# Optimization experiments

Measured on AMD Instinct MI355X. Metric: run time of the kernel, lower is better.

## Reference

```python
import jax, jax.numpy as jnp
import numpy as np
from jax import lax

V = 33          # n_vertices
B, H, W = 8, 1024, 1024
RES = 256       # backbone input resolution
N_FEATS = 128 * 8 * 8  # 8192


def setup_inputs() -> dict:
    key = jax.random.key(0)
    ks = jax.random.split(key, 16)
    inp = {"x": jax.random.uniform(ks[0], (B, 3, H, W), jnp.float32)}
    chans = [(3, 16), (16, 32), (32, 64), (64, 128), (128, 128)]
    for i, (ci, co) in enumerate(chans):
        inp[f"cw{i}"] = jax.random.normal(ks[1 + i], (co, ci, 3, 3), jnp.float32) / float(np.sqrt(ci * 9))
        inp[f"cb{i}"] = jnp.zeros((co,), jnp.float32)
    for i, c in enumerate([16, 32, 64, 128]):
        inp[f"g{i}"] = 1.0 + 0.02 * jax.random.normal(ks[6 + i], (c,), jnp.float32)  # InstanceNorm affine init
        inp[f"be{i}"] = jnp.zeros((c,), jnp.float32)
    inp["wg_w"] = 0.01 * jax.random.normal(ks[10], (3, N_FEATS), jnp.float32)
    inp["wg_b"] = jnp.ones((3,), jnp.float32)  # init_weights: ones bias
    # basis LUT bank: rank 0 = identity LUT (meshgrid, flip(0)), other ranks small noise
    grid = jnp.stack(jnp.meshgrid(*[jnp.arange(V, dtype=jnp.float32)] * 3, indexing="ij"), 0) / (V - 1)
    identity = jnp.flip(grid, 0).reshape(1, -1)          # [1, 3*V^3]
    rest = 0.01 * jax.random.normal(ks[11], (2, 3 * V ** 3), jnp.float32)
    inp["lut_w"] = jnp.concatenate([identity, rest], 0).T  # [3*V^3, n_ranks]
    inp["vertices"] = jnp.broadcast_to(jnp.arange(V, dtype=jnp.float32) / (V - 1), (3, V))[None]  # [1,3,V]
    return inp


def _conv(x, w, b, stride=2):
    y = lax.conv_general_dilated(x, w, (stride, stride), ((1, 1), (1, 1)),
                                 dimension_numbers=("NCHW", "OIHW", "NCHW"))
    return y + b[None, :, None, None]


def _inorm(x, g, be, eps=1e-5):
    m = x.mean((2, 3), keepdims=True)
    v = x.var((2, 3), keepdims=True)  # biased, matches torch InstanceNorm
    return (x - m) / jnp.sqrt(v + eps) * g[None, :, None, None] + be[None, :, None, None]


def _leaky(x):
    return jnp.where(x >= 0, x, 0.2 * x)


def _backbone(x, cws, cbs, gs, bes):
    h = jax.image.resize(x, (x.shape[0], 3, RES, RES), "bilinear")
    for i in range(4):  # Conv -> LeakyReLU -> InstanceNorm
        h = _inorm(_leaky(_conv(h, cws[i], cbs[i])), gs[i], bes[i])
    h = _leaky(_conv(h, cws[4], cbs[4]))  # last block, no norm; dropout = identity (eval)
    return h.reshape(x.shape[0], -1)


def _ailut(img, luts, vertices):
    # img [B,3,H,W], luts [B,3,V,V,V] (axes: out_ch, b, g, r), vertices [1,3,V]
    Bn, Vn = img.shape[0], vertices.shape[-1]
    verts = jnp.broadcast_to(vertices, (Bn, 3, Vn))
    q = img.reshape(Bn * 3, -1)
    vflat = verts.reshape(Bn * 3, Vn)
    idx = jax.vmap(lambda v, qq: jnp.searchsorted(v, qq, side="right"))(vflat, q) - 1
    idx = jnp.clip(idx, 0, Vn - 2).reshape(Bn, 3, -1)       # bin index per (b, color, pixel)
    lo = jnp.take_along_axis(verts, idx, axis=2)
    hi = jnp.take_along_axis(verts, idx + 1, axis=2)
    d = (img.reshape(Bn, 3, -1) - lo) / (hi - lo)           # fractional offset
    ir, ig, ib = idx[:, 0], idx[:, 1], idx[:, 2]
    dr, dg, db = d[:, 0], d[:, 1], d[:, 2]
    lflat = luts.reshape(Bn, 3, Vn ** 3)
    out = jnp.zeros_like(d)
    for ob in (0, 1):
        for og in (0, 1):
            for orr in (0, 1):
                w = ((db if ob else 1 - db) * (dg if og else 1 - dg) * (dr if orr else 1 - dr))
                lin = ((ib + ob) * Vn + (ig + og)) * Vn + (ir + orr)
                vals = jnp.take_along_axis(lflat, lin[:, None, :], axis=2)  # [B,3,N]
                out = out + w[:, None, :] * vals
    return out.reshape(img.shape)


def reference(x, cw0, cw1, cw2, cw3, cw4, cb0, cb1, cb2, cb3, cb4,
              g0, g1, g2, g3, be0, be1, be2, be3, wg_w, wg_b, lut_w, vertices):
    codes = _backbone(x, [cw0, cw1, cw2, cw3, cw4], [cb0, cb1, cb2, cb3, cb4],
                      [g0, g1, g2, g3], [be0, be1, be2, be3])   # [B, 8192]
    weights = codes @ wg_w.T + wg_b                              # [B, 3]
    luts = (weights @ lut_w.T).reshape(x.shape[0], 3, V, V, V)   # [B,3,V,V,V]
    outs = _ailut(x, luts, vertices)
    return outs, weights, luts, vertices
```

## Files before the change

kernel.cpp:

```cpp
#include <hip/hip_runtime.h>
#include <hip/hip_bf16.h>
#include <stdint.h>

typedef unsigned int U32;

static __device__ __forceinline__ U32 f2bf_rne(float f){
  U32 u; __builtin_memcpy(&u, &f, 4);
  u = (u + 0x7fffu + ((u >> 16) & 1u)) >> 16;
  return u & 0xffffu;
}
static __device__ __forceinline__ float bflo2f(U32 p){
  U32 u = p << 16; float f; __builtin_memcpy(&f, &u, 4); return f;
}
static __device__ __forceinline__ float bfhi2f(U32 p){
  U32 u = p & 0xffff0000u; float f; __builtin_memcpy(&f, &u, 4); return f;
}

__global__ void resize_k(const float* __restrict__ x, float* __restrict__ resz){
  __shared__ float hs[68][64];
  int blk = blockIdx.x;
  int tx = blk & 3;
  int ty = (blk >> 2) & 15;
  int bc = blk >> 6;
  int ox0 = tx << 6, oy0 = ty << 4;
  int r0 = 4*oy0 - 2; if (r0 < 0) r0 = 0;
  if (r0 > 956) r0 = 958;
  const float* src = x + ((size_t)bc << 20);
  int lane = threadIdx.x & 63;
  int wv   = threadIdx.x >> 6;
  int ox   = ox0 + lane;
  #pragma unroll 4
  for (int row = wv; row < 68; row += 4){
    int rr = r0 + row; if (rr > 1023) rr = 1023;
    const float4* row4 = (const float4*)(src + ((size_t)rr << 10));
    float4 f = row4[ox];
    float cprev = (3.f/32)*f.x + (1.f/32)*f.y;
    float cmid  = (5.f/32)*f.x + (7.f/32)*f.y + (7.f/32)*f.z + (5.f/32)*f.w;
    float cnext = (1.f/32)*f.z + (3.f/32)*f.w;
    float fromR = __shfl_down(cprev, 1, 64);
    float fromL = __shfl_up(cnext, 1, 64);
    if (lane == 63 && ox < 255){
      float4 h = row4[ox+1];
      fromR = (3.f/32)*h.x + (1.f/32)*h.y;
    }
    if (lane == 0 && ox > 0){
      float4 h = row4[ox-1];
      fromL = (1.f/32)*h.z + (3.f/32)*h.w;
    }
    float acc = fromL + cmid + fromR;
    if (ox == 0){
      float4 h1 = row4[1];
      acc = (0.625f/3.5f)*f.x + (0.875f/3.5f)*f.y
          + (0.875f/3.5f)*f.z + (0.625f/3.5f)*f.w
          + (0.375f/3.5f)*h1.x + (0.125f/3.5f)*h1.y;
    } else if (ox == 255){
      float4 h = row4[254];
      acc = (0.125f/3.5f)*h.z + (0.375f/3.5f)*h.w
          + (0.625f/3.5f)*f.x + (0.875f/3.5f)*f.y
          + (0.875f/3.5f)*f.z + (0.625f/3.5f)*f.w;
    }
    hs[row][lane] = acc;
  }
  __syncthreads();
  for (int i = threadIdx.x; i < 16*64; i += 256){
    int oyl = i >> 6, oxl = i & 63;
    int oy = oy0 + oyl;
    float acc;
    if (oy >= 1 && oy <= 254){
      int j0 = 4*oy - 2 - r0;
      acc = (1.f/32)*(hs[j0+0][oxl] + hs[j0+7][oxl])
          + (3.f/32)*(hs[j0+1][oxl] + hs[j0+6][oxl])
          + (5.f/32)*(hs[j0+2][oxl] + hs[j0+5][oxl])
          + (7.f/32)*(hs[j0+3][oxl] + hs[j0+4][oxl]);
    } else if (oy == 0){
      acc = (0.625f/3.5f)*hs[0][oxl] + (0.875f/3.5f)*hs[1][oxl]
          + (0.875f/3.5f)*hs[2][oxl] + (0.625f/3.5f)*hs[3][oxl]
          + (0.375f/3.5f)*hs[4][oxl] + (0.125f/3.5f)*hs[5][oxl];
    } else {
      int j0 = 1018 - r0;
      acc = (0.125f/3.5f)*hs[j0+0][oxl] + (0.375f/3.5f)*hs[j0+1][oxl]
          + (0.625f/3.5f)*hs[j0+2][oxl] + (0.875f/3.5f)*hs[j0+3][oxl]
          + (0.875f/3.5f)*hs[j0+4][oxl] + (0.625f/3.5f)*hs[j0+5][oxl];
    }
    resz[((size_t)bc << 16) + ((size_t)oy << 8) + (size_t)(ox0 + oxl)] = acc;
  }
}

__global__ void conv0_k(const float* __restrict__ in, const float* __restrict__ w,
                        const float* __restrict__ bias, float* __restrict__ out,
                        float* __restrict__ st0){
  __shared__ float tile[3][5][264];
  __shared__ float wsm[432];
  __shared__ float bs[16];
  __shared__ float sred[4][16][2];
  int t = blockIdx.x & 63;
  int b = blockIdx.x >> 6;
  for (int i = threadIdx.x; i < 432; i += 256) wsm[i] = w[i];
  if (threadIdx.x < 16) bs[threadIdx.x] = bias[threadIdx.x];
  const float* inb = in + (size_t)b*3*65536;
  int ih0 = 4*t - 1;
  for (int i = threadIdx.x; i < 3*5*258; i += 256){
    int ci  = i / (5*258);
    int rem = i % (5*258);
    int r   = rem / 258;
    int cc  = rem % 258;
    int ih  = ih0 + r;
    int iw  = cc - 1;
    float v = 0.f;
    if ((unsigned)ih < 256u && (unsigned)iw < 256u)
      v = inb[ci*65536 + ih*256 + iw];
    tile[ci][r][cc] = v;
  }
  __syncthreads();
  int lr = threadIdx.x >> 7;
  int ow = threadIdx.x & 127;
  float acc[16];
  #pragma unroll
  for (int j = 0; j < 16; j++) acc[j] = 0.f;
  #pragma unroll
  for (int ci = 0; ci < 3; ci++)
    #pragma unroll
    for (int kh = 0; kh < 3; kh++)
      #pragma unroll
      for (int kw = 0; kw < 3; kw++){
        float v = tile[ci][2*lr + kh][2*ow + kw];
        #pragma unroll
        for (int j = 0; j < 16; j++)
          acc[j] += v * wsm[j*27 + ci*9 + kh*3 + kw];
      }
  int s = t*256 + (int)threadIdx.x;
  size_t obase = (size_t)b*16*16384 + (size_t)s;
  float av[16];
  #pragma unroll
  for (int j = 0; j < 16; j++){
    float a = acc[j] + bs[j];
    a = (a >= 0.f) ? a : 0.2f*a;
    av[j] = a;
    out[obase + (size_t)j*16384] = a;
  }
  int wv = threadIdx.x >> 6;
  #pragma unroll
  for (int j = 0; j < 16; j++){
    float s1 = av[j], s2 = av[j]*av[j];
    #pragma unroll
    for (int o = 32; o > 0; o >>= 1){ s1 += __shfl_down(s1, o, 64); s2 += __shfl_down(s2, o, 64); }
    if ((threadIdx.x & 63) == 0){ sred[wv][j][0] = s1; sred[wv][j][1] = s2; }
  }
  __syncthreads();
  if (threadIdx.x < 16){
    float s1 = 0.f, s2 = 0.f;
    #pragma unroll
    for (int w2 = 0; w2 < 4; w2++){ s1 += sred[w2][threadIdx.x][0]; s2 += sred[w2][threadIdx.x][1]; }
    float* e = st0 + (((size_t)b*16 + threadIdx.x)*64 + t)*2;
    e[0] = s1; e[1] = s2;
  }
}

template<int CI, int CO, int IN, int OUT, int COB, int SPLIT, int TIN, int TOUT>
__global__ void __launch_bounds__(256, 1)
conv_leaky_k(const float* __restrict__ in, const float* __restrict__ w,
             const float* __restrict__ bias, float* __restrict__ out,
             const float* __restrict__ st_in, const float* __restrict__ g,
             const float* __restrict__ be, float* __restrict__ st_out){
  constexpr int P     = 256 / SPLIT;
  constexpr int TILES = (OUT*OUT + P - 1) / P;
  constexpr int NCB   = CO / COB;
  constexpr int CIS   = CI / SPLIT;
  constexpr int SUBS  = (TIN > 0) ? ((256/CI < TIN) ? 256/CI : TIN) : 1;
  int blk  = blockIdx.x;
  int b    = blk & 7;
  int rest = blk >> 3;
  int tile = rest % TILES;
  int cob  = rest / TILES;
  int co0  = cob * COB;
  __shared__ float ws[COB * CI * 9];
  __shared__ float bs[COB];
  __shared__ float red[(SPLIT > 1) ? 256 * COB : 1];
  __shared__ float sc[(TIN > 0) ? CI : 1];
  __shared__ float sh[(TIN > 0) ? CI : 1];
  __shared__ float pre[(TIN > 0) ? CI : 1][SUBS][2];
  for (int i = threadIdx.x; i < COB*CI*9; i += 256) ws[i] = w[(size_t)co0*CI*9 + i];
  if (threadIdx.x < COB) bs[threadIdx.x] = bias[co0 + threadIdx.x];
  if constexpr (TIN > 0){
    int c = threadIdx.x / SUBS, sub = threadIdx.x % SUBS;
    if (c < CI){
      const float* e = st_in + ((size_t)b*CI + c)*TIN*2;
      float s1 = 0.f, s2 = 0.f;
      for (int t2 = sub; t2 < TIN; t2 += SUBS){ s1 += e[t2*2]; s2 += e[t2*2+1]; }
      pre[c][sub][0] = s1; pre[c][sub][1] = s2;
    }
  }
  __syncthreads();
  if constexpr (TIN > 0){
    if (threadIdx.x < CI){
      float s1 = 0.f, s2 = 0.f;
      #pragma unroll
      for (int t2 = 0; t2 < SUBS; t2++){ s1 += pre[threadIdx.x][t2][0]; s2 += pre[threadIdx.x][t2][1]; }
      constexpr float hw = (float)(IN*IN);
      float mean = s1 * (1.f/hw);
      float var  = s2 * (1.f/hw) - mean*mean;
      float rstd = 1.f / sqrtf(var + 1e-5f);
      float scv  = g[threadIdx.x] * rstd;
      sc[threadIdx.x] = scv;
      sh[threadIdx.x] = be[threadIdx.x] - mean*scv;
    }
  }
  __syncthreads();
  int pix = threadIdx.x % P;
  int sp  = threadIdx.x / P;
  int s   = tile*P + pix;
  int oh = s / OUT, ow = s % OUT;
  float acc[COB];
  #pragma unroll
  for (int j = 0; j < COB; j++) acc[j] = 0.f;
  const float* inb = in + ((size_t)b*CI + sp*CIS) * (IN*IN);
  #pragma unroll
  for (int c0 = 0; c0 < CIS; c0 += 4){
    constexpr int CH = (CIS < 4) ? CIS : 4;
    #pragma unroll
    for (int kh = 0; kh < 3; kh++){
      int ih = oh*2 - 1 + kh;
      if ((unsigned)ih >= (unsigned)IN) continue;
      #pragma unroll
      for (int kw = 0; kw < 3; kw++){
        int iw = ow*2 - 1 + kw;
        if ((unsigned)iw >= (unsigned)IN) continue;
        const float* p0 = inb + (size_t)c0*(IN*IN) + ih*IN + iw;
        float vv[CH];
        #pragma unroll
        for (int ci = 0; ci < CH; ci++) vv[ci] = p0[(size_t)ci*(IN*IN)];
        if constexpr (TIN > 0){
          #pragma unroll
          for (int ci = 0; ci < CH; ci++) vv[ci] = vv[ci]*sc[sp*CIS+c0+ci] + sh[sp*CIS+c0+ci];
        }
        #pragma unroll
        for (int ci = 0; ci < CH; ci++){
          #pragma unroll
          for (int j = 0; j < COB; j++)
            acc[j] += vv[ci] * ws[j*CI*9 + (sp*CIS+c0+ci)*9 + kh*3 + kw];
        }
      }
    }
  }
  if constexpr (SPLIT > 1){
    #pragma unroll
    for (int j = 0; j < COB; j++) red[threadIdx.x*COB + j] = acc[j];
    __syncthreads();
    if (sp == 0){
      #pragma unroll
      for (int s2 = 1; s2 < SPLIT; s2++)
        #pragma unroll
        for (int j = 0; j < COB; j++)
          acc[j] += red[(pix + s2*P)*COB + j];
    }
  }
  float av[COB];
  if (sp == 0){
    size_t obase = ((size_t)b*CO + co0) * (size_t)(OUT*OUT) + s;
    #pragma unroll
    for (int j = 0; j < COB; j++){
      float a = acc[j] + bs[j];
      a = (a >= 0.f) ? a : 0.2f*a;
      av[j] = a;
      out[obase + (size_t)j*OUT*OUT] = a;
    }
  }
  if constexpr (TOUT > 0){
    constexpr int NW = P / 64;
    __shared__ float sred2[NW][COB][2];
    if (threadIdx.x < P){
      #pragma unroll
      for (int j = 0; j < COB; j++){
        float s1 = av[j], s2 = av[j]*av[j];
        #pragma unroll
        for (int o = 32; o > 0; o >>= 1){ s1 += __shfl_down(s1, o, 64); s2 += __shfl_down(s2, o, 64); }
        if ((threadIdx.x & 63) == 0){ int wv = threadIdx.x >> 6; sred2[wv][j][0] = s1; sred2[wv][j][1] = s2; }
      }
    }
    __syncthreads();
    if (threadIdx.x < COB){
      float s1 = 0.f, s2 = 0.f;
      #pragma unroll
      for (int wv = 0; wv < NW; wv++){ s1 += sred2[wv][threadIdx.x][0]; s2 += sred2[wv][threadIdx.x][1]; }
      float* e = st_out + (((size_t)b*CO + co0 + threadIdx.x)*TOUT + tile)*2;
      e[0] = s1; e[1] = s2;
    }
  }
}

static __device__ __forceinline__ float blockReduceSum256(float v, float* red){
  #pragma unroll
  for (int o = 32; o > 0; o >>= 1) v += __shfl_down(v, o, 64);
  __syncthreads();
  if ((threadIdx.x & 63) == 0) red[threadIdx.x >> 6] = v;
  __syncthreads();
  return red[0] + red[1] + red[2] + red[3];
}

__global__ void gemv_w_k(const float* __restrict__ codes, const float* __restrict__ wg_w,
                         const float* __restrict__ wg_b, float* __restrict__ wf,
                         float* __restrict__ outp){
  __shared__ float red[4];
  int b = blockIdx.x / 3, o = blockIdx.x % 3;
  const float* cp = codes + (size_t)b*8192;
  const float* wp = wg_w + (size_t)o*8192;
  float s = 0.f;
  for (int i = threadIdx.x; i < 8192; i += 256) s += cp[i] * wp[i];
  float tot = blockReduceSum256(s, red);
  if (threadIdx.x == 0){
    float v = tot + wg_b[o];
    wf[blockIdx.x] = v;
    outp[25165824 + blockIdx.x] = v;
  }
}

__global__ void luts_k(const float* __restrict__ wf, const float* __restrict__ lut_w,
                       const float* __restrict__ verts, U32* __restrict__ lp,
                       float* __restrict__ outp){
  int j = blockIdx.x * 256 + threadIdx.x;
  if (blockIdx.x == 0 && threadIdx.x < 99) outp[26028336 + threadIdx.x] = verts[threadIdx.x];
  if (j >= 107811) return;
  int jn = (j + 1 < 107811) ? (j + 1) : j;
  float l0 = lut_w[3*j+0], l1 = lut_w[3*j+1], l2 = lut_w[3*j+2];
  float m0 = lut_w[3*jn+0], m1 = lut_w[3*jn+1], m2 = lut_w[3*jn+2];
  int c = j / 35937;
  int i = j - c * 35937;
  #pragma unroll
  for (int b = 0; b < 8; b++){
    float w0 = wf[b*3+0], w1 = wf[b*3+1], w2 = wf[b*3+2];
    float v  = w0*l0 + w1*l1 + w2*l2;
    float vn = w0*m0 + w1*m1 + w2*m2;
    outp[25165848 + (size_t)b*107811 + j] = v;
    lp[(size_t)(b*3 + c)*35940 + i] = f2bf_rne(v) | (f2bf_rne(vn) << 16);
  }
}

static __device__ __forceinline__ void apply_phase(const U32* ls, const float4* rv,
                                                   const float4* gv, const float4* bv,
                                                   float* ob, int base){
  #pragma unroll
  for (int k = 0; k < 4; k++){
    float rr[4] = {rv[k].x, rv[k].y, rv[k].z, rv[k].w};
    float gg[4] = {gv[k].x, gv[k].y, gv[k].z, gv[k].w};
    float bb[4] = {bv[k].x, bv[k].y, bv[k].z, bv[k].w};
    U32 pw[4][4];
    float w00[4], w01[4], w10[4], w11[4], drx[4];
    #pragma unroll
    for (int h = 0; h < 4; h++){
      float rq = rr[h] * 32.f;
      float gq = gg[h] * 32.f;
      float bq = bb[h] * 32.f;
      int ir = (int)rq; ir = ir > 31 ? 31 : ir;
      int ig = (int)gq; ig = ig > 31 ? 31 : ig;
      int ib = (int)bq; ib = ib > 31 ? 31 : ib;
      float dr = rq - (float)ir;
      float dg = gq - (float)ig;
      float db = bq - (float)ib;
      int lin = (ib*33 + ig)*33 + ir;
      pw[h][0] = ls[lin];
      pw[h][1] = ls[lin+33];
      pw[h][2] = ls[lin+1089];
      pw[h][3] = ls[lin+1122];
      float t = db*dg;
      w11[h] = t;
      w10[h] = db - t;
      w01[h] = dg - t;
      w00[h] = 1.f - db - dg + t;
      drx[h] = dr;
    }
    float res[4];
    #pragma unroll
    for (int h = 0; h < 4; h++){
      float odr = 1.f - drx[h];
      float v0 = odr*bflo2f(pw[h][0]) + drx[h]*bfhi2f(pw[h][0]);
      float v1 = odr*bflo2f(pw[h][1]) + drx[h]*bfhi2f(pw[h][1]);
      float v2 = odr*bflo2f(pw[h][2]) + drx[h]*bfhi2f(pw[h][2]);
      float v3 = odr*bflo2f(pw[h][3]) + drx[h]*bfhi2f(pw[h][3]);
      res[h] = w00[h]*v0 + w01[h]*v1 + w10[h]*v2 + w11[h]*v3;
    }
    *(float4*)(ob + base + k*4096) = make_float4(res[0], res[1], res[2], res[3]);
  }
}

__global__ void __launch_bounds__(1024, 4) ailut_apply_k(const float* __restrict__ x,
                                                         const U32* __restrict__ lp,
                                                         float* __restrict__ outp){
  __shared__ U32 ls[35936];
  int b = blockIdx.z, c = blockIdx.y;
  const size_t plane = 1048576;
  const float* xb = x + (size_t)b*3*plane;
  int base = blockIdx.x * 32768 + (int)threadIdx.x*4;
  float4 rv[4], gv[4], bv[4];
  #pragma unroll
  for (int k = 0; k < 4; k++){
    int p0 = base + k*4096;
    rv[k] = *(const float4*)(xb + p0);
    gv[k] = *(const float4*)(xb + plane + p0);
    bv[k] = *(const float4*)(xb + 2*plane + p0);
  }
  const U32* lsrc = lp + (size_t)(b*3 + c)*35940;
  for (int i = threadIdx.x; i < 8984; i += 1024)
    __builtin_amdgcn_global_load_lds(
        (const __attribute__((address_space(1))) void*)(lsrc + 4*(size_t)i),
        (__attribute__((address_space(3))) void*)(ls + 4*i), 16, 0, 0);
  __syncthreads();
  float* ob = outp + ((size_t)b*3 + c)*plane;
  apply_phase(ls, rv, gv, bv, ob, base);
  #pragma unroll
  for (int k = 0; k < 4; k++){
    int p0 = base + 16384 + k*4096;
    rv[k] = *(const float4*)(xb + p0);
    gv[k] = *(const float4*)(xb + plane + p0);
    bv[k] = *(const float4*)(xb + 2*plane + p0);
  }
  apply_phase(ls, rv, gv, bv, ob, base + 16384);
}

extern "C" void kernel_launch(void* const* d_in, const int* in_sizes, int n_in,
                              void* d_out, int out_size, void* d_ws, size_t ws_size,
                              hipStream_t stream){
  const float* x    = (const float*)d_in[0];
  const float* cw0  = (const float*)d_in[1];
  const float* cb0  = (const float*)d_in[2];
  const float* cw1  = (const float*)d_in[3];
  const float* cb1  = (const float*)d_in[4];
  const float* cw2  = (const float*)d_in[5];
  const float* cb2  = (const float*)d_in[6];
  const float* cw3  = (const float*)d_in[7];
  const float* cb3  = (const float*)d_in[8];
  const float* cw4  = (const float*)d_in[9];
  const float* cb4  = (const float*)d_in[10];
  const float* g0   = (const float*)d_in[11];
  const float* be0  = (const float*)d_in[12];
  const float* g1   = (const float*)d_in[13];
  const float* be1  = (const float*)d_in[14];
  const float* g2   = (const float*)d_in[15];
  const float* be2  = (const float*)d_in[16];
  const float* g3   = (const float*)d_in[17];
  const float* be3  = (const float*)d_in[18];
  const float* wgw  = (const float*)d_in[19];
  const float* wgb  = (const float*)d_in[20];
  const float* lutw = (const float*)d_in[21];
  const float* vert = (const float*)d_in[22];
  float* out = (float*)d_out;
  float* ws  = (float*)d_ws;

  U32*   lp   = (U32*)ws;
  float* wf   = ws + 862592;
  float* st0  = ws + 862720;
  float* st1  = ws + 879104;
  float* st2  = ws + 887296;
  float* st3  = ws + 891392;
  float* resz = ws + 895488;
  float* act0 = ws + 2468352;
  float* act1 = act0 + 2097152;
  float* act2 = act1 + 1048576;
  float* act3 = act2 + 524288;
  float* act4 = act3 + 262144;

  resize_k<<<1536, 256, 0, stream>>>(x, resz);

  conv0_k<<<512, 256, 0, stream>>>(resz, cw0, cb0, act0, st0);
  conv_leaky_k<16,32,128,64,8,1,64,16>
      <<<8*4*16, 256, 0, stream>>>(act0, cw1, cb1, act1, st0, g0, be0, st1);
  conv_leaky_k<32,64,64,32,4,1,16,4>
      <<<8*16*4, 256, 0, stream>>>(act1, cw2, cb2, act2, st1, g1, be1, st2);
  conv_leaky_k<64,128,32,16,4,2,4,2>
      <<<8*32*2, 256, 0, stream>>>(act2, cw3, cb3, act3, st2, g2, be2, st3);
  conv_leaky_k<128,128,16,8,4,4,2,0>
      <<<8*32*1, 256, 0, stream>>>(act3, cw4, cb4, act4, st3, g3, be3, nullptr);

  gemv_w_k<<<24, 256, 0, stream>>>(act4, wgw, wgb, wf, out);
  luts_k<<<422, 256, 0, stream>>>(wf, lutw, vert, lp, out);
  ailut_apply_k<<<dim3(32,3,8), 1024, 0, stream>>>(x, lp, out);
}
```

Baseline: 195.0 us.

## Fuse backbone stages into one cooperative persistent kernel with grid syncs

Replaces the eight separate backbone kernel launches (resize, five convs, gemv, LUT generation) with a single cooperative kernel of 512 blocks that runs each stage in turn, separated by grid.sync(). Shared memory becomes one flat buffer carved per stage. The goal is to remove launch gaps and tail latency between the many small dependent kernels. In exchange it adds grid-wide barrier cost, caps parallelism at 512 blocks with launch bounds of 2 per CU (which may raise register pressure), and switches the conv channel loop to unroll 1.

```diff
diff --git a/kernel.cpp b/kernel.cpp
--- a/kernel.cpp
+++ b/kernel.cpp
@@ -1,7 +1,9 @@
 #include <hip/hip_runtime.h>
+#include <hip/hip_cooperative_groups.h>
 #include <hip/hip_bf16.h>
 #include <stdint.h>
 
+namespace cg = cooperative_groups;
 typedef unsigned int U32;
 
 static __device__ __forceinline__ U32 f2bf_rne(float f){
@@ -16,9 +18,20 @@
   U32 u = p & 0xffff0000u; float f; __builtin_memcpy(&f, &u, 4); return f;
 }
 
-__global__ void resize_k(const float* __restrict__ x, float* __restrict__ resz){
-  __shared__ float hs[68][64];
-  int blk = blockIdx.x;
+
+struct BArgs {
+  const float *x;
+  const float *cw0,*cb0,*cw1,*cb1,*cw2,*cb2,*cw3,*cb3,*cw4,*cb4;
+  const float *g0,*be0,*g1,*be1,*g2,*be2,*g3,*be3;
+  const float *wgw,*wgb,*lutw,*vert;
+  float *resz,*act0,*act1,*act2,*act3,*act4,*wf;
+  float *st0,*st1,*st2,*st3;
+  U32 *lp;
+  float *outp;
+};
+
+static __device__ void resize_stage(float* hs, int blk, const float* __restrict__ x,
+                                    float* __restrict__ resz){
   int tx = blk & 3;
   int ty = (blk >> 2) & 15;
   int bc = blk >> 6;
@@ -59,7 +72,7 @@
           + (0.625f/3.5f)*f.x + (0.875f/3.5f)*f.y
           + (0.875f/3.5f)*f.z + (0.625f/3.5f)*f.w;
     }
-    hs[row][lane] = acc;
+    hs[row*64 + lane] = acc;
   }
   __syncthreads();
   for (int i = threadIdx.x; i < 16*64; i += 256){
@@ -68,33 +81,34 @@
     float acc;
     if (oy >= 1 && oy <= 254){
       int j0 = 4*oy - 2 - r0;
-      acc = (1.f/32)*(hs[j0+0][oxl] + hs[j0+7][oxl])
-          + (3.f/32)*(hs[j0+1][oxl] + hs[j0+6][oxl])
-          + (5.f/32)*(hs[j0+2][oxl] + hs[j0+5][oxl])
-          + (7.f/32)*(hs[j0+3][oxl] + hs[j0+4][oxl]);
+      acc = (1.f/32)*(hs[(j0+0)*64+oxl] + hs[(j0+7)*64+oxl])
+          + (3.f/32)*(hs[(j0+1)*64+oxl] + hs[(j0+6)*64+oxl])
+          + (5.f/32)*(hs[(j0+2)*64+oxl] + hs[(j0+5)*64+oxl])
+          + (7.f/32)*(hs[(j0+3)*64+oxl] + hs[(j0+4)*64+oxl]);
     } else if (oy == 0){
-      acc = (0.625f/3.5f)*hs[0][oxl] + (0.875f/3.5f)*hs[1][oxl]
-          + (0.875f/3.5f)*hs[2][oxl] + (0.625f/3.5f)*hs[3][oxl]
-          + (0.375f/3.5f)*hs[4][oxl] + (0.125f/3.5f)*hs[5][oxl];
+      acc = (0.625f/3.5f)*hs[0*64+oxl] + (0.875f/3.5f)*hs[1*64+oxl]
+          + (0.875f/3.5f)*hs[2*64+oxl] + (0.625f/3.5f)*hs[3*64+oxl]
+          + (0.375f/3.5f)*hs[4*64+oxl] + (0.125f/3.5f)*hs[5*64+oxl];
     } else {
       int j0 = 1018 - r0;
-      acc = (0.125f/3.5f)*hs[j0+0][oxl] + (0.375f/3.5f)*hs[j0+1][oxl]
-          + (0.625f/3.5f)*hs[j0+2][oxl] + (0.875f/3.5f)*hs[j0+3][oxl]
-          + (0.875f/3.5f)*hs[j0+4][oxl] + (0.625f/3.5f)*hs[j0+5][oxl];
+      acc = (0.125f/3.5f)*hs[(j0+0)*64+oxl] + (0.375f/3.5f)*hs[(j0+1)*64+oxl]
+          + (0.625f/3.5f)*hs[(j0+2)*64+oxl] + (0.875f/3.5f)*hs[(j0+3)*64+oxl]
+          + (0.875f/3.5f)*hs[(j0+4)*64+oxl] + (0.625f/3.5f)*hs[(j0+5)*64+oxl];
     }
     resz[((size_t)bc << 16) + ((size_t)oy << 8) + (size_t)(ox0 + oxl)] = acc;
   }
-}
-
-__global__ void conv0_k(const float* __restrict__ in, const float* __restrict__ w,
-                        const float* __restrict__ bias, float* __restrict__ out,
-                        float* __restrict__ st0){
-  __shared__ float tile[3][5][264];
-  __shared__ float wsm[432];
-  __shared__ float bs[16];
-  __shared__ float sred[4][16][2];
-  int t = blockIdx.x & 63;
-  int b = blockIdx.x >> 6;
+  __syncthreads();
+}
+
+static __device__ void conv0_stage(float* smem, int blk, const float* __restrict__ in,
+                                   const float* __restrict__ w, const float* __restrict__ bias,
+                                   float* __restrict__ out, float* __restrict__ st0){
+  float* tile = smem;
+  float* wsm  = smem + 3960;
+  float* bs   = smem + 4392;
+  float* sred = smem + 4408;
+  int t = blk & 63;
+  int b = blk >> 6;
   for (int i = threadIdx.x; i < 432; i += 256) wsm[i] = w[i];
   if (threadIdx.x < 16) bs[threadIdx.x] = bias[threadIdx.x];
   const float* inb = in + (size_t)b*3*65536;
@@ -109,7 +123,7 @@
     float v = 0.f;
     if ((unsigned)ih < 256u && (unsigned)iw < 256u)
       v = inb[ci*65536 + ih*256 + iw];
-    tile[ci][r][cc] = v;
+    tile[(ci*5 + r)*264 + cc] = v;
   }
   __syncthreads();
   int lr = threadIdx.x >> 7;
@@ -123,7 +137,7 @@
     for (int kh = 0; kh < 3; kh++)
       #pragma unroll
       for (int kw = 0; kw < 3; kw++){
-        float v = tile[ci][2*lr + kh][2*ow + kw];
+        float v = tile[(ci*5 + 2*lr + kh)*264 + 2*ow + kw];
         #pragma unroll
         for (int j = 0; j < 16; j++)
           acc[j] += v * wsm[j*27 + ci*9 + kh*3 + kw];
@@ -144,41 +158,41 @@
     float s1 = av[j], s2 = av[j]*av[j];
     #pragma unroll
     for (int o = 32; o > 0; o >>= 1){ s1 += __shfl_down(s1, o, 64); s2 += __shfl_down(s2, o, 64); }
-    if ((threadIdx.x & 63) == 0){ sred[wv][j][0] = s1; sred[wv][j][1] = s2; }
+    if ((threadIdx.x & 63) == 0){ sred[(wv*16 + j)*2+0] = s1; sred[(wv*16 + j)*2+1] = s2; }
   }
   __syncthreads();
   if (threadIdx.x < 16){
     float s1 = 0.f, s2 = 0.f;
     #pragma unroll
-    for (int w2 = 0; w2 < 4; w2++){ s1 += sred[w2][threadIdx.x][0]; s2 += sred[w2][threadIdx.x][1]; }
+    for (int w2 = 0; w2 < 4; w2++){ s1 += sred[(w2*16 + threadIdx.x)*2]; s2 += sred[(w2*16 + threadIdx.x)*2+1]; }
     float* e = st0 + (((size_t)b*16 + threadIdx.x)*64 + t)*2;
     e[0] = s1; e[1] = s2;
   }
 }
 
 template<int CI, int CO, int IN, int OUT, int COB, int SPLIT, int TIN, int TOUT>
-__global__ void __launch_bounds__(256, 1)
-conv_leaky_k(const float* __restrict__ in, const float* __restrict__ w,
-             const float* __restrict__ bias, float* __restrict__ out,
-             const float* __restrict__ st_in, const float* __restrict__ g,
-             const float* __restrict__ be, float* __restrict__ st_out){
+static __device__ void conv_stage(float* smem, int blk,
+    const float* __restrict__ in, const float* __restrict__ w,
+    const float* __restrict__ bias, float* __restrict__ out,
+    const float* __restrict__ st_in, const float* __restrict__ g,
+    const float* __restrict__ be, float* __restrict__ st_out){
   constexpr int P     = 256 / SPLIT;
   constexpr int TILES = (OUT*OUT + P - 1) / P;
-  constexpr int NCB   = CO / COB;
   constexpr int CIS   = CI / SPLIT;
   constexpr int SUBS  = (TIN > 0) ? ((256/CI < TIN) ? 256/CI : TIN) : 1;
-  int blk  = blockIdx.x;
+  constexpr int NW    = P / 64;
+  float* ws  = smem;
+  float* bs  = ws + COB*CI*9;
+  float* red = bs + COB;
+  float* sc  = red + ((SPLIT > 1) ? 256*COB : 0);
+  float* sh  = sc + ((TIN > 0) ? CI : 0);
+  float* pre = sh + ((TIN > 0) ? CI : 0);
+  float* sr2 = pre + ((TIN > 0) ? CI*SUBS*2 : 0);
   int b    = blk & 7;
   int rest = blk >> 3;
   int tile = rest % TILES;
   int cob  = rest / TILES;
   int co0  = cob * COB;
-  __shared__ float ws[COB * CI * 9];
-  __shared__ float bs[COB];
-  __shared__ float red[(SPLIT > 1) ? 256 * COB : 1];
-  __shared__ float sc[(TIN > 0) ? CI : 1];
-  __shared__ float sh[(TIN > 0) ? CI : 1];
-  __shared__ float pre[(TIN > 0) ? CI : 1][SUBS][2];
   for (int i = threadIdx.x; i < COB*CI*9; i += 256) ws[i] = w[(size_t)co0*CI*9 + i];
   if (threadIdx.x < COB) bs[threadIdx.x] = bias[co0 + threadIdx.x];
   if constexpr (TIN > 0){
@@ -187,7 +201,7 @@
       const float* e = st_in + ((size_t)b*CI + c)*TIN*2;
       float s1 = 0.f, s2 = 0.f;
       for (int t2 = sub; t2 < TIN; t2 += SUBS){ s1 += e[t2*2]; s2 += e[t2*2+1]; }
-      pre[c][sub][0] = s1; pre[c][sub][1] = s2;
+      pre[(c*SUBS + sub)*2+0] = s1; pre[(c*SUBS + sub)*2+1] = s2;
     }
   }
   __syncthreads();
@@ -195,7 +209,10 @@
     if (threadIdx.x < CI){
       float s1 = 0.f, s2 = 0.f;
       #pragma unroll
-      for (int t2 = 0; t2 < SUBS; t2++){ s1 += pre[threadIdx.x][t2][0]; s2 += pre[threadIdx.x][t2][1]; }
+      for (int t2 = 0; t2 < SUBS; t2++){
+        s1 += pre[(threadIdx.x*SUBS + t2)*2];
+        s2 += pre[(threadIdx.x*SUBS + t2)*2+1];
+      }
       constexpr float hw = (float)(IN*IN);
       float mean = s1 * (1.f/hw);
       float var  = s2 * (1.f/hw) - mean*mean;
@@ -214,7 +231,7 @@
   #pragma unroll
   for (int j = 0; j < COB; j++) acc[j] = 0.f;
   const float* inb = in + ((size_t)b*CI + sp*CIS) * (IN*IN);
-  #pragma unroll
+  #pragma unroll 1
   for (int c0 = 0; c0 < CIS; c0 += 4){
     constexpr int CH = (CIS < 4) ? CIS : 4;
     #pragma unroll
@@ -266,59 +283,55 @@
     }
   }
   if constexpr (TOUT > 0){
-    constexpr int NW = P / 64;
-    __shared__ float sred2[NW][COB][2];
     if (threadIdx.x < P){
       #pragma unroll
       for (int j = 0; j < COB; j++){
         float s1 = av[j], s2 = av[j]*av[j];
         #pragma unroll
         for (int o = 32; o > 0; o >>= 1){ s1 += __shfl_down(s1, o, 64); s2 += __shfl_down(s2, o, 64); }
-        if ((threadIdx.x & 63) == 0){ int wv = threadIdx.x >> 6; sred2[wv][j][0] = s1; sred2[wv][j][1] = s2; }
+        if ((threadIdx.x & 63) == 0){
+          int wv = threadIdx.x >> 6;
+          sr2[(wv*COB + j)*2+0] = s1; sr2[(wv*COB + j)*2+1] = s2;
+        }
       }
     }
     __syncthreads();
     if (threadIdx.x < COB){
       float s1 = 0.f, s2 = 0.f;
       #pragma unroll
-      for (int wv = 0; wv < NW; wv++){ s1 += sred2[wv][threadIdx.x][0]; s2 += sred2[wv][threadIdx.x][1]; }
+      for (int wv = 0; wv < NW; wv++){ s1 += sr2[(wv*COB + threadIdx.x)*2]; s2 += sr2[(wv*COB + threadIdx.x)*2+1]; }
       float* e = st_out + (((size_t)b*CO + co0 + threadIdx.x)*TOUT + tile)*2;
       e[0] = s1; e[1] = s2;
     }
   }
 }
 
-static __device__ __forceinline__ float blockReduceSum256(float v, float* red){
-  #pragma unroll
-  for (int o = 32; o > 0; o >>= 1) v += __shfl_down(v, o, 64);
-  __syncthreads();
-  if ((threadIdx.x & 63) == 0) red[threadIdx.x >> 6] = v;
-  __syncthreads();
-  return red[0] + red[1] + red[2] + red[3];
-}
-
-__global__ void gemv_w_k(const float* __restrict__ codes, const float* __restrict__ wg_w,
-                         const float* __restrict__ wg_b, float* __restrict__ wf,
-                         float* __restrict__ outp){
-  __shared__ float red[4];
-  int b = blockIdx.x / 3, o = blockIdx.x % 3;
+static __device__ void gemv_stage(float* smem, int blk, const float* __restrict__ codes,
+                                  const float* __restrict__ wgw, const float* __restrict__ wgb,
+                                  float* __restrict__ wf, float* __restrict__ outp){
+  int b = blk / 3, o = blk % 3;
   const float* cp = codes + (size_t)b*8192;
-  const float* wp = wg_w + (size_t)o*8192;
+  const float* wp = wgw + (size_t)o*8192;
   float s = 0.f;
   for (int i = threadIdx.x; i < 8192; i += 256) s += cp[i] * wp[i];
-  float tot = blockReduceSum256(s, red);
+  #pragma unroll
+  for (int off = 32; off > 0; off >>= 1) s += __shfl_down(s, off, 64);
+  __syncthreads();
+  if ((threadIdx.x & 63) == 0) smem[threadIdx.x >> 6] = s;
+  __syncthreads();
+  float tot = smem[0] + smem[1] + smem[2] + smem[3];
   if (threadIdx.x == 0){
-    float v = tot + wg_b[o];
-    wf[blockIdx.x] = v;
-    outp[25165824 + blockIdx.x] = v;
-  }
-}
-
-__global__ void luts_k(const float* __restrict__ wf, const float* __restrict__ lut_w,
-                       const float* __restrict__ verts, U32* __restrict__ lp,
-                       float* __restrict__ outp){
-  int j = blockIdx.x * 256 + threadIdx.x;
-  if (blockIdx.x == 0 && threadIdx.x < 99) outp[26028336 + threadIdx.x] = verts[threadIdx.x];
+    float v = tot + wgb[o];
+    wf[blk] = v;
+    outp[25165824 + blk] = v;
+  }
+}
+
+static __device__ void luts_stage(int blk, const float* __restrict__ wf,
+                                  const float* __restrict__ lut_w, const float* __restrict__ verts,
+                                  U32* __restrict__ lp, float* __restrict__ outp){
+  int j = blk * 256 + threadIdx.x;
+  if (blk == 0 && threadIdx.x < 99) outp[26028336 + threadIdx.x] = verts[threadIdx.x];
   if (j >= 107811) return;
   int jn = (j + 1 < 107811) ? (j + 1) : j;
   float l0 = lut_w[3*j+0], l1 = lut_w[3*j+1], l2 = lut_w[3*j+2];
@@ -333,6 +346,39 @@
     outp[25165848 + (size_t)b*107811 + j] = v;
     lp[(size_t)(b*3 + c)*35940 + i] = f2bf_rne(v) | (f2bf_rne(vn) << 16);
   }
+}
+
+__global__ void __launch_bounds__(256, 2) backbone_k(BArgs a){
+  cg::grid_group grid = cg::this_grid();
+  __shared__ float smem[6656];
+  int blk = blockIdx.x;
+
+  for (int t = blk; t < 1536; t += 512)
+    resize_stage(smem, t, a.x, a.resz);
+  grid.sync();
+
+  conv0_stage(smem, blk, a.resz, a.cw0, a.cb0, a.act0, a.st0);
+  grid.sync();
+
+  conv_stage<16,32,128,64,8,1,64,16>(smem, blk, a.act0, a.cw1, a.cb1, a.act1, a.st0, a.g0, a.be0, a.st1);
+  grid.sync();
+
+  conv_stage<32,64,64,32,4,1,16,4>(smem, blk, a.act1, a.cw2, a.cb2, a.act2, a.st1, a.g1, a.be1, a.st2);
+  grid.sync();
+
+  conv_stage<64,128,32,16,4,2,4,2>(smem, blk, a.act2, a.cw3, a.cb3, a.act3, a.st2, a.g2, a.be2, a.st3);
+  grid.sync();
+
+  if (blk < 256)
+    conv_stage<128,128,16,8,4,4,2,0>(smem, blk, a.act3, a.cw4, a.cb4, a.act4, a.st3, a.g3, a.be3, nullptr);
+  grid.sync();
+
+  if (blk < 24)
+    gemv_stage(smem, blk, a.act4, a.wgw, a.wgb, a.wf, a.outp);
+  grid.sync();
+
+  if (blk < 422)
+    luts_stage(blk, a.wf, a.lutw, a.vert, a.lp, a.outp);
 }
 
 static __device__ __forceinline__ void apply_phase(const U32* ls, const float4* rv,
@@ -458,19 +504,21 @@
   float* act3 = act2 + 524288;
   float* act4 = act3 + 262144;
 
-  resize_k<<<1536, 256, 0, stream>>>(x, resz);
-
-  conv0_k<<<512, 256, 0, stream>>>(resz, cw0, cb0, act0, st0);
-  conv_leaky_k<16,32,128,64,8,1,64,16>
-      <<<8*4*16, 256, 0, stream>>>(act0, cw1, cb1, act1, st0, g0, be0, st1);
-  conv_leaky_k<32,64,64,32,4,1,16,4>
-      <<<8*16*4, 256, 0, stream>>>(act1, cw2, cb2, act2, st1, g1, be1, st2);
-  conv_leaky_k<64,128,32,16,4,2,4,2>
-      <<<8*32*2, 256, 0, stream>>>(act2, cw3, cb3, act3, st2, g2, be2, st3);
-  conv_leaky_k<128,128,16,8,4,4,2,0>
-      <<<8*32*1, 256, 0, stream>>>(act3, cw4, cb4, act4, st3, g3, be3, nullptr);
-
-  gemv_w_k<<<24, 256, 0, stream>>>(act4, wgw, wgb, wf, out);
-  luts_k<<<422, 256, 0, stream>>>(wf, lutw, vert, lp, out);
+  BArgs ba;
+  ba.x = x;
+  ba.cw0 = cw0; ba.cb0 = cb0; ba.cw1 = cw1; ba.cb1 = cb1;
+  ba.cw2 = cw2; ba.cb2 = cb2; ba.cw3 = cw3; ba.cb3 = cb3;
+  ba.cw4 = cw4; ba.cb4 = cb4;
+  ba.g0 = g0; ba.be0 = be0; ba.g1 = g1; ba.be1 = be1;
+  ba.g2 = g2; ba.be2 = be2; ba.g3 = g3; ba.be3 = be3;
+  ba.wgw = wgw; ba.wgb = wgb; ba.lutw = lutw; ba.vert = vert;
+  ba.resz = resz; ba.act0 = act0; ba.act1 = act1; ba.act2 = act2;
+  ba.act3 = act3; ba.act4 = act4; ba.wf = wf;
+  ba.st0 = st0; ba.st1 = st1; ba.st2 = st2; ba.st3 = st3;
+  ba.lp = lp; ba.outp = out;
+
+  void* kargs[] = { (void*)&ba };
+  hipLaunchCooperativeKernel((const void*)backbone_k, dim3(512), dim3(256), kargs, 0, stream);
+
   ailut_apply_k<<<dim3(32,3,8), 1024, 0, stream>>>(x, lp, out);
 }
```

Result: slower. 603.6 us (+209.6%).
